# Kernel optimization log

Measured on AMD Instinct MI355X. Metric: run time of the kernel, lower is better.

The kernel has to match this reference:

```python
import jax, jax.numpy as jnp
import numpy as np

N, L, H, E = 2, 2048, 8, 64
S = 2048
C_CLUSTERS = 256
ITERATIONS = 10
BITS = 32
TOPK = 32


def setup_inputs() -> dict:
    key = jax.random.key(0)
    k1, k2, k3, k4 = jax.random.split(key, 4)
    return {
        "queries": jax.random.normal(k1, (N, L, H, E), dtype=jnp.float32),
        "keys": jax.random.normal(k2, (N, S, H, E), dtype=jnp.float32),
        "values": jax.random.normal(k3, (N, S, H, E), dtype=jnp.float32),
        "planes": jax.random.normal(k4, (BITS, E + 1), dtype=jnp.float32),
    }


def _hash_bits(Q, planes):
    # Q: [N,H,L,E]; planes: [B, E+1] (last column is the hash bias)
    proj = jnp.einsum('nhle,be->nhlb', Q, planes[:, :-1]) + planes[:, -1]
    return (proj > 0).astype(jnp.float32)  # [N,H,L,B]


def _kmeans_hamming(hbits, n_clusters, iterations):
    # Lloyd iterations with hamming distance on the hash bit-vectors.
    n, h, l, b = hbits.shape
    init_idx = (jnp.arange(n_clusters) * l) // n_clusters
    cent = hbits[:, :, init_idx, :]  # [N,H,C,B], bits in {0,1}
    hsum = hbits.sum(-1)  # [N,H,L]

    def assign(cent):
        csum = cent.sum(-1)  # [N,H,C]
        # hamming(h,c) = sum_b h + sum_b c - 2 h.c for binary vectors
        dist = hsum[..., None] + csum[:, :, None, :] \
            - 2.0 * jnp.einsum('nhlb,nhcb->nhlc', hbits, cent)
        return jnp.argmin(dist, axis=-1)  # [N,H,L]

    def body(cent, _):
        a = assign(cent)
        oh = jax.nn.one_hot(a, n_clusters, dtype=jnp.float32)  # [N,H,L,C]
        counts = oh.sum(2)  # [N,H,C]
        sums = jnp.einsum('nhlc,nhlb->nhcb', oh, hbits)
        new = (sums / jnp.maximum(counts, 1.0)[..., None] >= 0.5).astype(jnp.float32)
        cent = jnp.where(counts[..., None] > 0, new, cent)  # keep empty centroids
        return cent, None

    cent, _ = jax.lax.scan(body, cent, None, length=iterations)
    a = assign(cent)
    oh = jax.nn.one_hot(a, n_clusters, dtype=jnp.float32)
    counts = oh.sum(2)
    return a, counts, oh


def reference(queries, keys, values, planes):
    Q = jnp.transpose(queries, (0, 2, 1, 3))  # [N,H,L,E]
    K = jnp.transpose(keys, (0, 2, 1, 3))     # [N,H,S,E]
    V = jnp.transpose(values, (0, 2, 1, 3))   # [N,H,S,E]
    n, h, l, e = Q.shape
    t = 1.0 / jnp.sqrt(jnp.asarray(e, jnp.float32))

    # --- hash & cluster queries (non-differentiable routing) ---
    hbits = _hash_bits(jax.lax.stop_gradient(Q), planes)
    clusters, counts, oh = _kmeans_hamming(hbits, C_CLUSTERS, ITERATIONS)

    # --- group queries: per-cluster mean (=_GroupQueries) ---
    safe = jnp.maximum(counts, 1.0)
    Qg = jnp.einsum('nhlc,nhle->nhce', oh, Q) / safe[..., None]  # [N,H,C,E]

    QK = jnp.einsum('nhce,nhse->nhcs', Qg, K)  # [N,H,C,S]; key mask is all zeros
    topv, topi = jax.lax.top_k(QK, TOPK)       # [N,H,C,k]

    # --- bottom-k attention (full softmax with top-k zeroed) ---
    A = jax.nn.softmax(t * QK, axis=-1)
    n_i = jnp.arange(n)[:, None, None, None]
    h_i = jnp.arange(h)[None, :, None, None]
    c_i = jnp.arange(C_CLUSTERS)[None, None, :, None]
    A_masked = A.at[n_i, h_i, c_i, topi].set(0.0)
    A_bk = A_masked.sum(-1)  # [N,H,C]
    Vg = jnp.einsum('nhcs,nhse->nhce', A_masked, V)  # [N,H,C,E]
    V_bottom = jnp.take_along_axis(Vg, clusters[..., None], axis=2)  # broadcast -> [N,H,L,E]
    A_bk_q = jnp.take_along_axis(A_bk, clusters, axis=2)  # [N,H,L]

    # --- top-k attention recomputed per query with its cluster's top-k keys ---
    top_q = jnp.take_along_axis(topi, clusters[..., None], axis=2)  # [N,H,L,k]
    idx = top_q.reshape(n, h, l * TOPK)[..., None]
    Kq = jnp.take_along_axis(K, idx, axis=2).reshape(n, h, l, TOPK, e)
    QKt = jnp.einsum('nhle,nhlke->nhlk', Q, Kq)
    At = jax.nn.softmax(t * QKt, axis=-1) * (1.0 - A_bk_q)[..., None]
    Vq = jnp.take_along_axis(V, idx, axis=2).reshape(n, h, l, TOPK, e)
    V_top = jnp.einsum('nhlk,nhlke->nhle', At, Vq)

    out = V_top + V_bottom  # [N,H,L,E]
    return jnp.transpose(out, (0, 2, 1, 3))  # [N,L,H,E]
```

## Files before the change

### kernel.cpp

```cpp
#include <hip/hip_runtime.h>
#include <math.h>
#include <float.h>

#define NB 2
#define LQ 2048
#define HH 8
#define EE 64
#define SS 2048
#define CC 256
#define KM_ITERS 10
#define NBITS 32
#define TK 32
#define NH (NB*HH)
#define CG 4

__global__ __launch_bounds__(256) void k_hash(const float* __restrict__ Q,
                                              const float* __restrict__ planes,
                                              unsigned int* __restrict__ qmask) {
    int gid = blockIdx.x * 256 + threadIdx.x;
    int nh = gid >> 11, l = gid & (LQ - 1);
    int n = nh >> 3, h = nh & 7;
    const float* qrow = Q + (((size_t)n * LQ + l) * HH + h) * EE;
    float q[64];
    #pragma unroll
    for (int e = 0; e < 64; e++) q[e] = qrow[e];
    unsigned int m = 0;
    for (int b = 0; b < NBITS; b++) {
        double acc = (double)planes[b * 65 + 64];
        #pragma unroll
        for (int e = 0; e < 64; e++) acc += (double)q[e] * (double)planes[b * 65 + e];
        if (acc > 0.0) m |= (1u << b);
    }
    qmask[gid] = m;
}

__global__ __launch_bounds__(256) void k_cinit(const unsigned int* __restrict__ qmask,
                                               unsigned int* __restrict__ cent_g) {
    int nh = blockIdx.x, t = threadIdx.x;
    cent_g[nh * CC + t] = qmask[(size_t)nh * LQ + t * 8];
}

__global__ __launch_bounds__(256) void k_assign(const unsigned int* __restrict__ qmask,
                                                const unsigned int* __restrict__ cent_g,
                                                int* __restrict__ asg) {
    int nh = blockIdx.x >> 3;
    int p = ((blockIdx.x & 7) << 8) + threadIdx.x;
    int t = threadIdx.x;
    __shared__ __align__(16) unsigned int cent[CC];
    cent[t] = cent_g[nh * CC + t];
    __syncthreads();
    unsigned int m = qmask[(size_t)nh * LQ + p];
    int best = 0x7fffffff;
    const uint4* c4p = (const uint4*)cent;
    #pragma unroll 4
    for (int c4 = 0; c4 < CC / 4; c4++) {
        uint4 cm = c4p[c4];
        int base = c4 << 2;
        int e0 = (__popc(m ^ cm.x) << 8) + base;
        int e1 = (__popc(m ^ cm.y) << 8) + base + 1;
        int e2 = (__popc(m ^ cm.z) << 8) + base + 2;
        int e3 = (__popc(m ^ cm.w) << 8) + base + 3;
        int e01 = e0 < e1 ? e0 : e1;
        int e23 = e2 < e3 ? e2 : e3;
        int e = e01 < e23 ? e01 : e23;
        best = best < e ? best : e;
    }
    asg[(size_t)nh * LQ + p] = best & 255;
}

__global__ __launch_bounds__(512) void k_update(const unsigned int* __restrict__ qmask,
                                                const int* __restrict__ asg,
                                                unsigned int* __restrict__ cent_g) {
    int nh = blockIdx.x, t = threadIdx.x;
    __shared__ unsigned int sorted[LQ];
    __shared__ int cnts[CC], offs[CC], cursor[CC];
    if (t < CC) cnts[t] = 0;
    int bc[4]; unsigned int mym[4];
    #pragma unroll
    for (int k = 0; k < 4; k++) {
        bc[k] = asg[(size_t)nh * LQ + t + k * 512];
        mym[k] = qmask[(size_t)nh * LQ + t + k * 512];
    }
    __syncthreads();
    #pragma unroll
    for (int k = 0; k < 4; k++) atomicAdd(&cnts[bc[k]], 1);
    __syncthreads();
    if (t < 64) {
        int c0 = cnts[4 * t], c1 = cnts[4 * t + 1], c2 = cnts[4 * t + 2], c3 = cnts[4 * t + 3];
        int s1 = c0 + c1, s2 = s1 + c2, tot = s2 + c3;
        int inc = tot;
        #pragma unroll
        for (int o = 1; o < 64; o <<= 1) {
            int v = __shfl_up(inc, o);
            if (t >= o) inc += v;
        }
        int excl = inc - tot;
        offs[4 * t] = excl;          cursor[4 * t] = excl;
        offs[4 * t + 1] = excl + c0; cursor[4 * t + 1] = excl + c0;
        offs[4 * t + 2] = excl + s1; cursor[4 * t + 2] = excl + s1;
        offs[4 * t + 3] = excl + s2; cursor[4 * t + 3] = excl + s2;
    }
    __syncthreads();
    int cl = t >> 1, j = t & 1;
    int cnt_c = cnts[cl], off_c = offs[cl];
    #pragma unroll
    for (int k = 0; k < 4; k++) {
        int pos = atomicAdd(&cursor[bc[k]], 1);
        sorted[pos] = mym[k];
    }
    __syncthreads();
    int bs[32];
    #pragma unroll
    for (int b = 0; b < 32; b++) bs[b] = 0;
    for (int i = j; i < cnt_c; i += 2) {
        unsigned int m = sorted[off_c + i];
        #pragma unroll
        for (int b = 0; b < 32; b++) bs[b] += (m >> b) & 1;
    }
    #pragma unroll
    for (int b = 0; b < 32; b++) bs[b] += __shfl_xor(bs[b], 1);
    if (j == 0 && cnt_c > 0) {
        unsigned int nc = 0;
        #pragma unroll
        for (int b = 0; b < 32; b++) if (2 * bs[b] >= cnt_c) nc |= (1u << b);
        cent_g[nh * CC + cl] = nc;
    }
}

__global__ __launch_bounds__(512) void k_finalize(const int* __restrict__ asg,
                                                  int* __restrict__ counts_out,
                                                  int* __restrict__ order_out,
                                                  int* __restrict__ offsets_out) {
    int nh = blockIdx.x, t = threadIdx.x;
    __shared__ int cnts[CC], offs[CC], cursor[CC];
    if (t < CC) cnts[t] = 0;
    int bc[4];
    #pragma unroll
    for (int k = 0; k < 4; k++) bc[k] = asg[(size_t)nh * LQ + t + k * 512];
    __syncthreads();
    #pragma unroll
    for (int k = 0; k < 4; k++) atomicAdd(&cnts[bc[k]], 1);
    __syncthreads();
    if (t < 64) {
        int c0 = cnts[4 * t], c1 = cnts[4 * t + 1], c2 = cnts[4 * t + 2], c3 = cnts[4 * t + 3];
        int s1 = c0 + c1, s2 = s1 + c2, tot = s2 + c3;
        int inc = tot;
        #pragma unroll
        for (int o = 1; o < 64; o <<= 1) {
            int v = __shfl_up(inc, o);
            if (t >= o) inc += v;
        }
        int excl = inc - tot;
        offs[4 * t] = excl;          cursor[4 * t] = excl;
        offs[4 * t + 1] = excl + c0; cursor[4 * t + 1] = excl + c0;
        offs[4 * t + 2] = excl + s1; cursor[4 * t + 2] = excl + s1;
        offs[4 * t + 3] = excl + s2; cursor[4 * t + 3] = excl + s2;
    }
    __syncthreads();
    if (t < CC) {
        counts_out[nh * CC + t] = cnts[t];
        offsets_out[nh * CC + t] = offs[t];
    }
    #pragma unroll
    for (int k = 0; k < 4; k++) {
        int pos = atomicAdd(&cursor[bc[k]], 1);
        order_out[(size_t)nh * LQ + pos] = t + k * 512;
    }
}

__global__ __launch_bounds__(256) void k_qg(const float* __restrict__ Q,
                                            const int* __restrict__ order,
                                            const int* __restrict__ offsets,
                                            const int* __restrict__ counts,
                                            double* __restrict__ Qg) {
    int nh = blockIdx.x >> 6;
    int c = (blockIdx.x & 63) * 4 + (threadIdx.x >> 6);
    int e = threadIdx.x & 63;
    int n = nh >> 3, h = nh & 7;
    int off = offsets[nh * CC + c];
    int cnt = counts[nh * CC + c];
    const int* ord = order + (size_t)nh * LQ + off;
    double acc = 0.0;
    for (int i = 0; i < cnt; i++) {
        int p = ord[i];
        acc += (double)Q[(((size_t)n * LQ + p) * HH + h) * EE + e];
    }
    double safe = cnt > 0 ? (double)cnt : 1.0;
    Qg[((size_t)(nh * CC + c)) * EE + e] = acc / safe;
}

__global__ __launch_bounds__(256) void k_transpose(const float* __restrict__ Xp,
                                                   float* __restrict__ Xt) {
    int nh = blockIdx.x >> 5;
    int s0 = (blockIdx.x & 31) * 64;
    int n = nh >> 3, h = nh & 7;
    __shared__ float tile[64][65];
    int t = threadIdx.x;
    int e = t & 63, r0 = t >> 6;
    #pragma unroll
    for (int j = 0; j < 16; j++) {
        int r = r0 * 16 + j;
        tile[r][e] = Xp[(((size_t)n * SS + s0 + r) * HH + h) * EE + e];
    }
    __syncthreads();
    int sl = t & 63, eg = t >> 6;
    #pragma unroll
    for (int j = 0; j < 16; j++) {
        int ee_ = eg * 16 + j;
        Xt[((size_t)nh * EE + ee_) * SS + s0 + sl] = tile[sl][ee_];
    }
}

__global__ __launch_bounds__(256) void k_rows(const float* __restrict__ Kt,
                                              const float* __restrict__ Vt,
                                              const double* __restrict__ Qg,
                                              int* __restrict__ topi,
                                              float* __restrict__ abk,
                                              float* __restrict__ Vg) {
    int bid = blockIdx.x;
    int xcd = bid & 7, idx = bid >> 3;
    int nh = xcd * 2 + (idx >> 6);
    int cg = idx & 63;
    int c0 = cg * CG;
    int t = threadIdx.x, w = t >> 6, l = t & 63;

    __shared__ double qgl[EE][CG];
    __shared__ float pred[CG][EE][17];

    qgl[t >> 2][t & 3] = Qg[((size_t)(nh * CC + c0 + (t & 3))) * EE + (t >> 2)];
    __syncthreads();

    double v[32];
    #pragma unroll
    for (int k = 0; k < 32; k++) v[k] = 0.0;
    const float* ktb = Kt + ((size_t)nh * EE) * SS + l * 4;
    for (int e = 0; e < EE; e++) {
        double qe = qgl[e][w];
        const float4* kr = (const float4*)(ktb + (size_t)e * SS);
        #pragma unroll
        for (int kb = 0; kb < 8; kb++) {
            float4 kv = kr[kb * 64];
            v[4 * kb + 0] += qe * (double)kv.x;
            v[4 * kb + 1] += qe * (double)kv.y;
            v[4 * kb + 2] += qe * (double)kv.z;
            v[4 * kb + 3] += qe * (double)kv.w;
        }
    }

    double m = v[0];
    #pragma unroll
    for (int k = 1; k < 32; k++) m = v[k] > m ? v[k] : m;
    #pragma unroll
    for (int o = 32; o > 0; o >>= 1) { double z = __shfl_xor(m, o); m = z > m ? z : m; }

    double ds = 0.0;
    #pragma unroll
    for (int k = 0; k < 32; k++) ds += (double)expf(0.125f * (float)(v[k] - m));
    #pragma unroll
    for (int o = 32; o > 0; o >>= 1) ds += __shfl_xor(ds, o);

    unsigned ext = 0u;
    double lbv = -1e301; int lbi = 1 << 30;
    #pragma unroll
    for (int k = 0; k < 32; k++)
        if (v[k] > lbv) { lbv = v[k]; lbi = ((k >> 2) << 8) + l * 4 + (k & 3); }
    double topsum = 0.0;
    int rowid = nh * CC + c0 + w;
    for (int kk = 0; kk < TK; kk++) {
        double bv = lbv; int bi = lbi;
        #pragma unroll
        for (int o = 32; o > 0; o >>= 1) {
            double v2 = __shfl_xor(bv, o); int i2 = __shfl_xor(bi, o);
            if (v2 > bv || (v2 == bv && i2 < bi)) { bv = v2; bi = i2; }
        }
        topsum += (double)expf(0.125f * (float)(bv - m));
        if (l == 0) topi[(size_t)rowid * TK + kk] = bi;
        if (((bi >> 2) & 63) == l) {
            ext |= 1u << (((bi >> 8) << 2) | (bi & 3));
            lbv = -1e301; lbi = 1 << 30;
            #pragma unroll
            for (int k = 0; k < 32; k++)
                if (!((ext >> k) & 1) && v[k] > lbv) { lbv = v[k]; lbi = ((k >> 2) << 8) + l * 4 + (k & 3); }
        }
    }
    if (l == 0) abk[rowid] = (float)((ds - topsum) / ds);

    float invd = (float)(1.0 / ds);
    float w32[32];
    #pragma unroll
    for (int k = 0; k < 32; k++)
        w32[k] = ((ext >> k) & 1) ? 0.0f
               : expf(0.125f * (float)(v[k] - m)) * invd;

    const float* vtb = Vt + ((size_t)nh * EE) * SS + l * 4;
    for (int e = 0; e < EE; e++) {
        const float4* vr = (const float4*)(vtb + (size_t)e * SS);
        float a0 = 0.f, a1 = 0.f, a2 = 0.f, a3 = 0.f;
        #pragma unroll
        for (int kb = 0; kb < 8; kb += 4) {
            float4 v0 = vr[kb * 64], v1 = vr[(kb + 1) * 64], v2 = vr[(kb + 2) * 64], v3 = vr[(kb + 3) * 64];
            a0 += w32[4 * kb + 0] * v0.x + w32[4 * kb + 1] * v0.y + w32[4 * kb + 2] * v0.z + w32[4 * kb + 3] * v0.w;
            a1 += w32[4 * kb + 4] * v1.x + w32[4 * kb + 5] * v1.y + w32[4 * kb + 6] * v1.z + w32[4 * kb + 7] * v1.w;
            a2 += w32[4 * kb + 8] * v2.x + w32[4 * kb + 9] * v2.y + w32[4 * kb + 10] * v2.z + w32[4 * kb + 11] * v2.w;
            a3 += w32[4 * kb + 12] * v3.x + w32[4 * kb + 13] * v3.y + w32[4 * kb + 14] * v3.z + w32[4 * kb + 15] * v3.w;
        }
        float acc = (a0 + a1) + (a2 + a3);
        acc += __shfl_xor(acc, 16);
        acc += __shfl_xor(acc, 32);
        if (l < 16) pred[w][e][l] = acc;
    }
    __syncthreads();
    {
        int c = t >> 6, e = t & 63;
        float s = 0.f;
        #pragma unroll
        for (int i = 0; i < 16; i++) s += pred[c][e][i];
        Vg[((size_t)(nh * CC + c0 + c)) * EE + e] = s;
    }
}

__global__ __launch_bounds__(256) void k_out(const float* __restrict__ Q,
                                             const float* __restrict__ Kp,
                                             const float* __restrict__ Vp,
                                             const int* __restrict__ clusters,
                                             const int* __restrict__ topi,
                                             const float* __restrict__ abk,
                                             const float* __restrict__ Vg,
                                             float* __restrict__ out) {
    int tid = threadIdx.x, wid = tid >> 6, e = tid & 63;
    int q = blockIdx.x * 4 + wid;
    int nh = q >> 11, l = q & (LQ - 1);
    int n = nh >> 3, h = nh & 7;
    int c = clusters[q];
    float scale = 1.0f - abk[nh * CC + c];
    const int* ti = topi + (size_t)(nh * CC + c) * TK;
    float qe = Q[(((size_t)n * LQ + l) * HH + h) * EE + e];
    float myv = -INFINITY;
    for (int k = 0; k < TK; k++) {
        int idx = ti[k];
        float kv = Kp[(((size_t)n * SS + idx) * HH + h) * EE + e];
        float v = qe * kv;
        #pragma unroll
        for (int o = 32; o > 0; o >>= 1) v += __shfl_xor(v, o);
        if (e == k) myv = v;
    }
    float mv = myv;
    #pragma unroll
    for (int o = 32; o > 0; o >>= 1) { float v = __shfl_xor(mv, o); mv = v > mv ? v : mv; }
    float p = (e < TK) ? expf(0.125f * (myv - mv)) : 0.0f;
    float ssum = p;
    #pragma unroll
    for (int o = 32; o > 0; o >>= 1) ssum += __shfl_xor(ssum, o);
    float at = p / ssum * scale;
    float acc = 0.0f;
    for (int k = 0; k < TK; k++) {
        float wk = __shfl(at, k, 64);
        int idx = ti[k];
        acc += wk * Vp[(((size_t)n * SS + idx) * HH + h) * EE + e];
    }
    acc += Vg[(size_t)(nh * CC + c) * EE + e];
    out[(((size_t)n * LQ + l) * HH + h) * EE + e] = acc;
}

extern "C" void kernel_launch(void* const* d_in, const int* in_sizes, int n_in,
                              void* d_out, int out_size, void* d_ws, size_t ws_size,
                              hipStream_t stream) {
    const float* Q      = (const float*)d_in[0];
    const float* K      = (const float*)d_in[1];
    const float* V      = (const float*)d_in[2];
    const float* planes = (const float*)d_in[3];
    float* out = (float*)d_out;

    char* ws = (char*)d_ws;
    unsigned int* qmask    = (unsigned int*)(ws);
    int*          clusters = (int*)(ws + (128 << 10));
    int*          counts   = (int*)(ws + (256 << 10));
    float*        abk      = (float*)(ws + (272 << 10));
    int*          topi     = (int*)(ws + (288 << 10));
    float*        Vg       = (float*)(ws + (800 << 10));
    double*       Qg       = (double*)(ws + (1824 << 10));
    float*        Kt       = (float*)(ws + (4096 << 10));
    int*          order    = (int*)(ws + (12288 << 10));
    int*          offsets  = (int*)(ws + (12416 << 10));
    unsigned int* cent_g   = (unsigned int*)(ws + (12432 << 10));
    float*        Vt       = (float*)(ws + (12544 << 10));

    k_transpose<<<dim3(NH * 32), dim3(256), 0, stream>>>(K, Kt);
    k_transpose<<<dim3(NH * 32), dim3(256), 0, stream>>>(V, Vt);
    k_hash<<<dim3(NH * LQ / 256), dim3(256), 0, stream>>>(Q, planes, qmask);
    k_cinit<<<dim3(NH), dim3(256), 0, stream>>>(qmask, cent_g);
    for (int it = 0; it < KM_ITERS; ++it) {
        k_assign<<<dim3(NH * 8), dim3(256), 0, stream>>>(qmask, cent_g, clusters);
        k_update<<<dim3(NH), dim3(512), 0, stream>>>(qmask, clusters, cent_g);
    }
    k_assign<<<dim3(NH * 8), dim3(256), 0, stream>>>(qmask, cent_g, clusters);
    k_finalize<<<dim3(NH), dim3(512), 0, stream>>>(clusters, counts, order, offsets);
    k_qg<<<dim3(NH * 64), dim3(256), 0, stream>>>(Q, order, offsets, counts, Qg);
    k_rows<<<dim3(NH * CC / CG), dim3(256), 0, stream>>>(Kt, Vt, Qg, topi, abk, Vg);
    k_out<<<dim3(NH * LQ / 4), dim3(256), 0, stream>>>(Q, K, V, clusters, topi, abk, Vg, out);
}
```

Before: 468.5 us.

## Compute cluster-key scores in fp32 with fp64 fallback near top-k boundary

The cluster-query by key score accumulation in k_rows moves from fp64 to fp32. A new kernel computes each head's maximum key norm, which sets an error bound eps. Rows whose gap between the 32nd and 33rd scores falls below that bound redo the whole computation in fp64, so top-k selection stays consistent with the reference. This removes the slow fp64 FMA path for most rows, at the cost of an extra kernel, a memset, per-row divergence for ambiguous rows, and a launch-bounds occupancy hint.

Measured after the change: 525.6 us. 12.2% more time.

```diff
diff --git a/kernel.cpp b/kernel.cpp
--- a/kernel.cpp
+++ b/kernel.cpp
@@ -211,12 +211,34 @@
     }
 }
 
-__global__ __launch_bounds__(256) void k_rows(const float* __restrict__ Kt,
-                                              const float* __restrict__ Vt,
-                                              const double* __restrict__ Qg,
-                                              int* __restrict__ topi,
-                                              float* __restrict__ abk,
-                                              float* __restrict__ Vg) {
+__global__ __launch_bounds__(512) void k_knorm(const float* __restrict__ Kt,
+                                               unsigned int* __restrict__ Knorm2) {
+    int nh = blockIdx.x >> 2;
+    int s = ((blockIdx.x & 3) << 9) + threadIdx.x;
+    const float* kc = Kt + ((size_t)nh * EE) * SS + s;
+    float acc = 0.f;
+    for (int e = 0; e < EE; e++) { float kv = kc[(size_t)e * SS]; acc += kv * kv; }
+    #pragma unroll
+    for (int o = 32; o > 0; o >>= 1) { float z = __shfl_xor(acc, o); acc = z > acc ? z : acc; }
+    __shared__ float red[8];
+    int w = threadIdx.x >> 6, l = threadIdx.x & 63;
+    if (l == 0) red[w] = acc;
+    __syncthreads();
+    if (threadIdx.x == 0) {
+        float m = red[0];
+        #pragma unroll
+        for (int i = 1; i < 8; i++) m = red[i] > m ? red[i] : m;
+        atomicMax(&Knorm2[nh], __float_as_uint(m));
+    }
+}
+
+__global__ __launch_bounds__(256, 4) void k_rows(const float* __restrict__ Kt,
+                                                 const float* __restrict__ Vt,
+                                                 const double* __restrict__ Qg,
+                                                 const unsigned int* __restrict__ Knorm2,
+                                                 int* __restrict__ topi,
+                                                 float* __restrict__ abk,
+                                                 float* __restrict__ Vg) {
     int bid = blockIdx.x;
     int xcd = bid & 7, idx = bid >> 3;
     int nh = xcd * 2 + (idx >> 6);
@@ -225,89 +247,179 @@
     int t = threadIdx.x, w = t >> 6, l = t & 63;
 
     __shared__ double qgl[EE][CG];
-    __shared__ float pred[CG][EE][17];
-
-    qgl[t >> 2][t & 3] = Qg[((size_t)(nh * CC + c0 + (t & 3))) * EE + (t >> 2)];
-    __syncthreads();
-
-    double v[32];
-    #pragma unroll
-    for (int k = 0; k < 32; k++) v[k] = 0.0;
+    __shared__ float  qglf[EE][CG];
+    __shared__ float  pred[CG][EE][17];
+
+    {
+        double qv = Qg[((size_t)(nh * CC + c0 + (t & 3))) * EE + (t >> 2)];
+        qgl[t >> 2][t & 3] = qv;
+        qglf[t >> 2][t & 3] = (float)qv;
+    }
+    __syncthreads();
+
+    float v[32];
+    #pragma unroll
+    for (int k = 0; k < 32; k++) v[k] = 0.f;
     const float* ktb = Kt + ((size_t)nh * EE) * SS + l * 4;
-    for (int e = 0; e < EE; e++) {
-        double qe = qgl[e][w];
-        const float4* kr = (const float4*)(ktb + (size_t)e * SS);
-        #pragma unroll
-        for (int kb = 0; kb < 8; kb++) {
-            float4 kv = kr[kb * 64];
-            v[4 * kb + 0] += qe * (double)kv.x;
-            v[4 * kb + 1] += qe * (double)kv.y;
-            v[4 * kb + 2] += qe * (double)kv.z;
-            v[4 * kb + 3] += qe * (double)kv.w;
-        }
-    }
-
-    double m = v[0];
-    #pragma unroll
-    for (int k = 1; k < 32; k++) m = v[k] > m ? v[k] : m;
-    #pragma unroll
-    for (int o = 32; o > 0; o >>= 1) { double z = __shfl_xor(m, o); m = z > m ? z : m; }
-
-    double ds = 0.0;
-    #pragma unroll
-    for (int k = 0; k < 32; k++) ds += (double)expf(0.125f * (float)(v[k] - m));
+    {
+        const float4* kr = (const float4*)ktb;
+        for (int e = 0; e < EE; e++) {
+            float qe = qglf[e][w];
+            #pragma unroll
+            for (int kb = 0; kb < 8; kb++) {
+                float4 kv = kr[kb * 64];
+                v[4 * kb + 0] += qe * kv.x;
+                v[4 * kb + 1] += qe * kv.y;
+                v[4 * kb + 2] += qe * kv.z;
+                v[4 * kb + 3] += qe * kv.w;
+            }
+            kr += SS / 4;
+        }
+    }
+
+    float mf = v[0];
+    #pragma unroll
+    for (int k = 1; k < 32; k++) mf = v[k] > mf ? v[k] : mf;
+    #pragma unroll
+    for (int o = 32; o > 0; o >>= 1) { float z = __shfl_xor(mf, o); mf = z > mf ? z : mf; }
+
+    float ds = 0.f;
+    #pragma unroll
+    for (int k = 0; k < 32; k++) ds += expf(0.125f * (v[k] - mf));
     #pragma unroll
     for (int o = 32; o > 0; o >>= 1) ds += __shfl_xor(ds, o);
 
     unsigned ext = 0u;
-    double lbv = -1e301; int lbi = 1 << 30;
+    float lbv = -3.0e38f; int lbi = 1 << 30;
     #pragma unroll
     for (int k = 0; k < 32; k++)
         if (v[k] > lbv) { lbv = v[k]; lbi = ((k >> 2) << 8) + l * 4 + (k & 3); }
-    double topsum = 0.0;
+    float topsum = 0.f, s32 = 0.f;
     int rowid = nh * CC + c0 + w;
     for (int kk = 0; kk < TK; kk++) {
-        double bv = lbv; int bi = lbi;
+        float bv = lbv; int bi = lbi;
         #pragma unroll
         for (int o = 32; o > 0; o >>= 1) {
-            double v2 = __shfl_xor(bv, o); int i2 = __shfl_xor(bi, o);
+            float v2 = __shfl_xor(bv, o); int i2 = __shfl_xor(bi, o);
             if (v2 > bv || (v2 == bv && i2 < bi)) { bv = v2; bi = i2; }
         }
-        topsum += (double)expf(0.125f * (float)(bv - m));
+        topsum += expf(0.125f * (bv - mf));
         if (l == 0) topi[(size_t)rowid * TK + kk] = bi;
+        if (kk == TK - 1) s32 = bv;
         if (((bi >> 2) & 63) == l) {
             ext |= 1u << (((bi >> 8) << 2) | (bi & 3));
-            lbv = -1e301; lbi = 1 << 30;
+            lbv = -3.0e38f; lbi = 1 << 30;
             #pragma unroll
             for (int k = 0; k < 32; k++)
                 if (!((ext >> k) & 1) && v[k] > lbv) { lbv = v[k]; lbi = ((k >> 2) << 8) + l * 4 + (k & 3); }
         }
     }
-    if (l == 0) abk[rowid] = (float)((ds - topsum) / ds);
-
-    float invd = (float)(1.0 / ds);
+    float s33;
+    {
+        float bv = lbv; int bi = lbi;
+        #pragma unroll
+        for (int o = 32; o > 0; o >>= 1) {
+            float v2 = __shfl_xor(bv, o); int i2 = __shfl_xor(bi, o);
+            if (v2 > bv || (v2 == bv && i2 < bi)) { bv = v2; bi = i2; }
+        }
+        s33 = bv;
+    }
+    float qn2;
+    {
+        float qv = qglf[l][w];
+        qn2 = qv * qv;
+        #pragma unroll
+        for (int o = 32; o > 0; o >>= 1) qn2 += __shfl_xor(qn2, o);
+    }
+    float kn2 = __uint_as_float(Knorm2[nh]);
+    float eps2 = 1.6e-5f * sqrtf(qn2 * kn2);
+
     float w32[32];
-    #pragma unroll
-    for (int k = 0; k < 32; k++)
-        w32[k] = ((ext >> k) & 1) ? 0.0f
-               : expf(0.125f * (float)(v[k] - m)) * invd;
+    if (s32 - s33 < eps2) {
+        double v64[32];
+        #pragma unroll
+        for (int k = 0; k < 32; k++) v64[k] = 0.0;
+        const float4* kr = (const float4*)ktb;
+        for (int e = 0; e < EE; e++) {
+            double qe = qgl[e][w];
+            #pragma unroll
+            for (int kb = 0; kb < 8; kb++) {
+                float4 kv = kr[kb * 64];
+                v64[4 * kb + 0] += qe * (double)kv.x;
+                v64[4 * kb + 1] += qe * (double)kv.y;
+                v64[4 * kb + 2] += qe * (double)kv.z;
+                v64[4 * kb + 3] += qe * (double)kv.w;
+            }
+            kr += SS / 4;
+        }
+        double m64 = v64[0];
+        #pragma unroll
+        for (int k = 1; k < 32; k++) m64 = v64[k] > m64 ? v64[k] : m64;
+        #pragma unroll
+        for (int o = 32; o > 0; o >>= 1) { double z = __shfl_xor(m64, o); m64 = z > m64 ? z : m64; }
+        double ds64 = 0.0;
+        #pragma unroll
+        for (int k = 0; k < 32; k++) ds64 += (double)expf(0.125f * (float)(v64[k] - m64));
+        #pragma unroll
+        for (int o = 32; o > 0; o >>= 1) ds64 += __shfl_xor(ds64, o);
+        unsigned ex2 = 0u;
+        double lb = -1e301; int li = 1 << 30;
+        #pragma unroll
+        for (int k = 0; k < 32; k++)
+            if (v64[k] > lb) { lb = v64[k]; li = ((k >> 2) << 8) + l * 4 + (k & 3); }
+        double ts64 = 0.0;
+        for (int kk = 0; kk < TK; kk++) {
+            double bv = lb; int bi = li;
+            #pragma unroll
+            for (int o = 32; o > 0; o >>= 1) {
+                double v2 = __shfl_xor(bv, o); int i2 = __shfl_xor(bi, o);
+                if (v2 > bv || (v2 == bv && i2 < bi)) { bv = v2; bi = i2; }
+            }
+            ts64 += (double)expf(0.125f * (float)(bv - m64));
+            if (l == 0) topi[(size_t)rowid * TK + kk] = bi;
+            if (((bi >> 2) & 63) == l) {
+                ex2 |= 1u << (((bi >> 8) << 2) | (bi & 3));
+                lb = -1e301; li = 1 << 30;
+                #pragma unroll
+                for (int k = 0; k < 32; k++)
+                    if (!((ex2 >> k) & 1) && v64[k] > lb) { lb = v64[k]; li = ((k >> 2) << 8) + l * 4 + (k & 3); }
+            }
+        }
+        if (l == 0) abk[rowid] = (float)((ds64 - ts64) / ds64);
+        float invd = (float)(1.0 / ds64);
+        #pragma unroll
+        for (int k = 0; k < 32; k++)
+            w32[k] = ((ex2 >> k) & 1) ? 0.0f
+                   : expf(0.125f * (float)(v64[k] - m64)) * invd;
+    } else {
+        if (l == 0) abk[rowid] = (ds - topsum) / ds;
+        float invd = 1.0f / ds;
+        #pragma unroll
+        for (int k = 0; k < 32; k++)
+            w32[k] = ((ext >> k) & 1) ? 0.0f
+                   : expf(0.125f * (v[k] - mf)) * invd;
+    }
 
     const float* vtb = Vt + ((size_t)nh * EE) * SS + l * 4;
-    for (int e = 0; e < EE; e++) {
-        const float4* vr = (const float4*)(vtb + (size_t)e * SS);
-        float a0 = 0.f, a1 = 0.f, a2 = 0.f, a3 = 0.f;
-        #pragma unroll
-        for (int kb = 0; kb < 8; kb += 4) {
-            float4 v0 = vr[kb * 64], v1 = vr[(kb + 1) * 64], v2 = vr[(kb + 2) * 64], v3 = vr[(kb + 3) * 64];
-            a0 += w32[4 * kb + 0] * v0.x + w32[4 * kb + 1] * v0.y + w32[4 * kb + 2] * v0.z + w32[4 * kb + 3] * v0.w;
-            a1 += w32[4 * kb + 4] * v1.x + w32[4 * kb + 5] * v1.y + w32[4 * kb + 6] * v1.z + w32[4 * kb + 7] * v1.w;
-            a2 += w32[4 * kb + 8] * v2.x + w32[4 * kb + 9] * v2.y + w32[4 * kb + 10] * v2.z + w32[4 * kb + 11] * v2.w;
-            a3 += w32[4 * kb + 12] * v3.x + w32[4 * kb + 13] * v3.y + w32[4 * kb + 14] * v3.z + w32[4 * kb + 15] * v3.w;
-        }
-        float acc = (a0 + a1) + (a2 + a3);
-        acc += __shfl_xor(acc, 16);
-        acc += __shfl_xor(acc, 32);
-        if (l < 16) pred[w][e][l] = acc;
+    {
+        const float4* vrb = (const float4*)vtb;
+        for (int e = 0; e < EE; e++) {
+            const float4* vr = vrb;
+            float a0 = 0.f, a1 = 0.f, a2 = 0.f, a3 = 0.f;
+            #pragma unroll
+            for (int kb = 0; kb < 8; kb += 4) {
+                float4 v0 = vr[kb * 64], v1 = vr[(kb + 1) * 64], v2 = vr[(kb + 2) * 64], v3 = vr[(kb + 3) * 64];
+                a0 += w32[4 * kb + 0] * v0.x + w32[4 * kb + 1] * v0.y + w32[4 * kb + 2] * v0.z + w32[4 * kb + 3] * v0.w;
+                a1 += w32[4 * kb + 4] * v1.x + w32[4 * kb + 5] * v1.y + w32[4 * kb + 6] * v1.z + w32[4 * kb + 7] * v1.w;
+                a2 += w32[4 * kb + 8] * v2.x + w32[4 * kb + 9] * v2.y + w32[4 * kb + 10] * v2.z + w32[4 * kb + 11] * v2.w;
+                a3 += w32[4 * kb + 12] * v3.x + w32[4 * kb + 13] * v3.y + w32[4 * kb + 14] * v3.z + w32[4 * kb + 15] * v3.w;
+            }
+            float acc = (a0 + a1) + (a2 + a3);
+            acc += __shfl_xor(acc, 16);
+            acc += __shfl_xor(acc, 32);
+            if (l < 16) pred[w][e][l] = acc;
+            vrb += SS / 4;
+        }
     }
     __syncthreads();
     {
@@ -383,10 +495,13 @@
     int*          order    = (int*)(ws + (12288 << 10));
     int*          offsets  = (int*)(ws + (12416 << 10));
     unsigned int* cent_g   = (unsigned int*)(ws + (12432 << 10));
+    unsigned int* Knorm2   = (unsigned int*)(ws + (12448 << 10));
     float*        Vt       = (float*)(ws + (12544 << 10));
 
+    hipMemsetAsync(Knorm2, 0, NH * sizeof(unsigned int), stream);
     k_transpose<<<dim3(NH * 32), dim3(256), 0, stream>>>(K, Kt);
     k_transpose<<<dim3(NH * 32), dim3(256), 0, stream>>>(V, Vt);
+    k_knorm<<<dim3(NH * 4), dim3(512), 0, stream>>>(Kt, Knorm2);
     k_hash<<<dim3(NH * LQ / 256), dim3(256), 0, stream>>>(Q, planes, qmask);
     k_cinit<<<dim3(NH), dim3(256), 0, stream>>>(qmask, cent_g);
     for (int it = 0; it < KM_ITERS; ++it) {
@@ -396,6 +511,6 @@
     k_assign<<<dim3(NH * 8), dim3(256), 0, stream>>>(qmask, cent_g, clusters);
     k_finalize<<<dim3(NH), dim3(512), 0, stream>>>(clusters, counts, order, offsets);
     k_qg<<<dim3(NH * 64), dim3(256), 0, stream>>>(Q, order, offsets, counts, Qg);
-    k_rows<<<dim3(NH * CC / CG), dim3(256), 0, stream>>>(Kt, Vt, Qg, topi, abk, Vg);
+    k_rows<<<dim3(NH * CC / CG), dim3(256), 0, stream>>>(Kt, Vt, Qg, Knorm2, topi, abk, Vg);
     k_out<<<dim3(NH * LQ / 4), dim3(256), 0, stream>>>(Q, K, V, clusters, topi, abk, Vg, out);
 }
```
